# Optimization experiments

Hardware: AMD Instinct MI355X
Metric: run time of the kernel (lower is better)

The kernel has to match this reference:

```python
import jax, jax.numpy as jnp
import numpy as np
import math

D_MODEL = 2048
NUM_HEADS = 16
D_FF = 8192
HEAD_DIM = D_MODEL // NUM_HEADS
EPS = 1e-5


def _xavier(key, out_f, in_f):
    std = math.sqrt(2.0 / (in_f + out_f))
    return jax.random.normal(key, (out_f, in_f), dtype=jnp.float32) * std


def setup_inputs() -> dict:
    key = jax.random.key(0)
    ks = jax.random.split(key, 8)
    x = jax.random.normal(ks[0], (2, 2048, D_MODEL), dtype=jnp.float32)
    return {
        "x": x,
        "Wq": _xavier(ks[1], D_MODEL, D_MODEL),
        "Wk": _xavier(ks[2], D_MODEL, D_MODEL),
        "Wv": _xavier(ks[3], D_MODEL, D_MODEL),
        "Wo": _xavier(ks[4], D_MODEL, D_MODEL),
        "W1": _xavier(ks[5], D_FF, D_MODEL),
        "W2": _xavier(ks[6], D_MODEL, D_FF),
        "g1": jnp.ones((D_MODEL,), jnp.float32),
        "b1": jnp.zeros((D_MODEL,), jnp.float32),
        "g2": jnp.ones((D_MODEL,), jnp.float32),
        "b2": jnp.zeros((D_MODEL,), jnp.float32),
    }


def _ternary(w):
    # per-tensor abs-mean threshold -> {-1, 0, 1}
    abs_w = jnp.abs(w)
    thr = jnp.mean(abs_w)
    return jnp.where(abs_w > thr, jnp.sign(w), jnp.zeros_like(w))


def _tlin(x, w):
    # F.linear with ternarized weight [out, in], no bias
    return jnp.einsum("bsi,oi->bso", x, _ternary(w))


def _layernorm(x, g, b):
    mu = jnp.mean(x, axis=-1, keepdims=True)
    var = jnp.mean(jnp.square(x - mu), axis=-1, keepdims=True)
    return (x - mu) * jax.lax.rsqrt(var + EPS) * g + b


def reference(x, Wq, Wk, Wv, Wo, W1, W2, g1, b1, g2, b2):
    B, S, D = x.shape
    H, Hd = NUM_HEADS, HEAD_DIM
    q = _tlin(x, Wq).reshape(B, S, H, Hd).transpose(0, 2, 1, 3)  # bhsd
    k = _tlin(x, Wk).reshape(B, S, H, Hd).transpose(0, 2, 1, 3)
    v = _tlin(x, Wv).reshape(B, S, H, Hd).transpose(0, 2, 1, 3)
    scores = jnp.einsum("bhqd,bhkd->bhqk", q, k) / math.sqrt(Hd)
    probs = jax.nn.softmax(scores, axis=-1)
    attn = jnp.einsum("bhqk,bhkd->bhqd", probs, v)
    attn = attn.transpose(0, 2, 1, 3).reshape(B, S, D)
    attn = _tlin(attn, Wo)
    x = _layernorm(x + attn, g1, b1)  # dropout is identity in eval
    ff = _tlin(jax.nn.relu(_tlin(x, W1)), W2)
    x = _layernorm(x + ff, g2, b2)
    return x
```

## Files before the change

kernel.cpp:

```cpp
#include <hip/hip_runtime.h>
#include <hip/hip_bf16.h>

typedef __bf16 bf16_t;
typedef __bf16 bf16x8 __attribute__((ext_vector_type(8)));
typedef __bf16 bf16x4 __attribute__((ext_vector_type(4)));
typedef float f32x4 __attribute__((ext_vector_type(4)));
typedef int i32x4 __attribute__((ext_vector_type(4)));

__device__ __forceinline__ f32x4 mfma16(bf16x8 a, bf16x8 b, f32x4 c) {
  return __builtin_amdgcn_mfma_f32_16x16x32_bf16(a, b, c, 0, 0, 0);
}

__device__ __forceinline__ void gload16(const void* g, void* l) {
  __builtin_amdgcn_global_load_lds(
      (const __attribute__((address_space(1))) void*)g,
      (__attribute__((address_space(3))) void*)l, 16, 0, 0);
}

__global__ void abssum_all(const float* __restrict__ W0, const float* __restrict__ W1_,
                           const float* __restrict__ W2_, const float* __restrict__ W3,
                           const float* __restrict__ W4, const float* __restrict__ W5,
                           double* __restrict__ partial) {
  __shared__ double sd[256];
  const int w = blockIdx.y, tid = threadIdx.x;
  const float* W = (w == 0) ? W0 : (w == 1) ? W1_ : (w == 2) ? W2_ : (w == 3) ? W3 : (w == 4) ? W4 : W5;
  const int n4 = (w < 4) ? 1048576 : 4194304;
  double s = 0.0;
  for (int i = blockIdx.x * 256 + tid; i < n4; i += 262144) {
    float4 v = ((const float4*)W)[i];
    s += (double)fabsf(v.x); s += (double)fabsf(v.y);
    s += (double)fabsf(v.z); s += (double)fabsf(v.w);
  }
  sd[tid] = s; __syncthreads();
  for (int st = 128; st > 0; st >>= 1) { if (tid < st) sd[tid] += sd[tid + st]; __syncthreads(); }
  if (tid == 0) partial[w * 1024 + blockIdx.x] = sd[0];
}

__global__ void abssum_fin(const double* __restrict__ partial, double* __restrict__ sums) {
  __shared__ double sd[256];
  const int tid = threadIdx.x;
  const double* p = partial + blockIdx.x * 1024;
  double s = p[tid] + p[tid + 256] + p[tid + 512] + p[tid + 768];
  sd[tid] = s; __syncthreads();
  for (int st = 128; st > 0; st >>= 1) { if (tid < st) sd[tid] += sd[tid + st]; __syncthreads(); }
  if (tid == 0) sums[blockIdx.x] = sd[0];
}

__global__ void ternarize_k(const float* __restrict__ W, bf16_t* __restrict__ out,
                            const double* __restrict__ sum, double n) {
  const double thr = sum[0] / n;
  const int i = blockIdx.x * 256 + threadIdx.x;
  float4 v = ((const float4*)W)[i];
  bf16x4 o;
  float t;
  t = ((double)fabsf(v.x) > thr) ? (v.x > 0.f ? 1.f : -1.f) : 0.f; o[0] = (bf16_t)t;
  t = ((double)fabsf(v.y) > thr) ? (v.y > 0.f ? 1.f : -1.f) : 0.f; o[1] = (bf16_t)t;
  t = ((double)fabsf(v.z) > thr) ? (v.z > 0.f ? 1.f : -1.f) : 0.f; o[2] = (bf16_t)t;
  t = ((double)fabsf(v.w) > thr) ? (v.w > 0.f ? 1.f : -1.f) : 0.f; o[3] = (bf16_t)t;
  *(bf16x4*)&out[(size_t)i * 4] = o;
}

__global__ void split_x_k(const float* __restrict__ X, bf16_t* __restrict__ xh, bf16_t* __restrict__ xl) {
  const int i = blockIdx.x * 256 + threadIdx.x;
  float4 v = ((const float4*)X)[i];
  bf16x4 h, l;
  h[0] = (bf16_t)v.x; l[0] = (bf16_t)(v.x - (float)h[0]);
  h[1] = (bf16_t)v.y; l[1] = (bf16_t)(v.y - (float)h[1]);
  h[2] = (bf16_t)v.z; l[2] = (bf16_t)(v.z - (float)h[2]);
  h[3] = (bf16_t)v.w; l[3] = (bf16_t)(v.w - (float)h[3]);
  *(bf16x4*)&xh[(size_t)i * 4] = h;
  *(bf16x4*)&xl[(size_t)i * 4] = l;
}

template <int EPI, bool SPLITA>
__global__ __launch_bounds__(512, 2) void gemmP(
    const bf16_t* __restrict__ Ah, const bf16_t* __restrict__ Al,
    const bf16_t* __restrict__ Bw,
    void* __restrict__ C0, void* __restrict__ C1,
    int M, int N, int K) {
  constexpr int BM = SPLITA ? 64 : 128;
  constexpr int MREP = SPLITA ? 2 : 4;
  constexpr int ABUF = BM * 64;
  constexpr int BBUF = 256 * 64;
  __shared__ __align__(16) bf16_t sA[3][ABUF];
  __shared__ __align__(16) bf16_t sA2[SPLITA ? 3 : 1][SPLITA ? ABUF : 8];
  __shared__ __align__(16) bf16_t sB[3][BBUF];

  const int tid = threadIdx.x;
  const int wid = tid >> 6, lane = tid & 63, lr = lane & 15, lg = lane >> 4;
  const int wr = wid >> 2, wc = wid & 3;
  const size_t Ks = (size_t)K;

  const int nwg = gridDim.x * gridDim.y;
  const int bid0 = blockIdx.y * gridDim.x + blockIdx.x;
  const int swz = (bid0 & 7) * (nwg >> 3) + (bid0 >> 3);
  const int bx = swz % gridDim.x, by = swz / gridDim.x;
  const size_t m0 = (size_t)by * BM, n0 = (size_t)bx * 256;
  const int nt = K / 64;

  f32x4 acc[MREP][4] = {};

  auto STAGEH = [&](int bi, int kt, int half) {
    const size_t ko = (size_t)kt * 64;
    if (half == 0) {
#pragma unroll
      for (int i = 0; i < BM / 64; i++) {
        const int t = i * 512 + tid;
        const int r = t >> 3;
        const int su = (t & 7) ^ (r & 7);
        const int lo = (i * 512 + wid * 64) * 8;
        gload16(Ah + (m0 + r) * Ks + ko + su * 8, (void*)&sA[bi][lo]);
        if constexpr (SPLITA) gload16(Al + (m0 + r) * Ks + ko + su * 8, (void*)&sA2[bi][lo]);
      }
      {
        const int r = tid >> 3;
        const int su = (tid & 7) ^ (r & 7);
        gload16(Bw + (n0 + r) * Ks + ko + su * 8, (void*)&sB[bi][(wid * 64) * 8]);
      }
    } else {
#pragma unroll
      for (int i = 1; i < 4; i++) {
        const int t = i * 512 + tid;
        const int r = t >> 3;
        const int su = (t & 7) ^ (r & 7);
        gload16(Bw + (n0 + r) * Ks + ko + su * 8, (void*)&sB[bi][(i * 512 + wid * 64) * 8]);
      }
    }
  };
  auto LDA = [&](const bf16_t* base, int m, int k) -> bf16x8 {
    const int row = wr * (BM / 2) + m * 16 + lr;
    const int u = (k * 4 + lg) ^ (lr & 7);
    return *(const bf16x8*)&base[row * 64 + u * 8];
  };
  auto LDB = [&](const bf16_t* base, int n, int k) -> bf16x8 {
    const int row = wc * 64 + n * 16 + lr;
    const int u = (k * 4 + lg) ^ (lr & 7);
    return *(const bf16x8*)&base[row * 64 + u * 8];
  };

  STAGEH(0, 0, 0); STAGEH(0, 0, 1);
  STAGEH(1, 1, 0); STAGEH(1, 1, 1);
  asm volatile("s_waitcnt vmcnt(6)" ::: "memory");
  __builtin_amdgcn_s_barrier();

  int bc = 0, bs = 2;
  for (int kt = 0; kt < nt; kt++) {
    const bool pf = (kt + 2 < nt);
    bf16x8 a[MREP][2], bfr[4][2];
#pragma unroll
    for (int m = 0; m < MREP; m++)
#pragma unroll
      for (int k = 0; k < 2; k++) a[m][k] = LDA(&sA[bc][0], m, k);
    if constexpr (SPLITA) {
#pragma unroll
      for (int n = 0; n < 4; n++)
#pragma unroll
        for (int k = 0; k < 2; k++) bfr[n][k] = LDB(&sB[bc][0], n, k);
    } else {
#pragma unroll
      for (int n = 0; n < 2; n++)
#pragma unroll
        for (int k = 0; k < 2; k++) bfr[n][k] = LDB(&sB[bc][0], n, k);
    }
    if (pf) STAGEH(bs, kt + 2, 0);
    __builtin_amdgcn_s_barrier();
    asm volatile("s_waitcnt lgkmcnt(0)" ::: "memory");
    __builtin_amdgcn_sched_barrier(0);
    __builtin_amdgcn_s_setprio(1);
    if constexpr (SPLITA) {
#pragma unroll
      for (int k = 0; k < 2; k++)
#pragma unroll
        for (int m = 0; m < MREP; m++)
#pragma unroll
          for (int n = 0; n < 4; n++) acc[m][n] = mfma16(a[m][k], bfr[n][k], acc[m][n]);
    } else {
#pragma unroll
      for (int k = 0; k < 2; k++)
#pragma unroll
        for (int m = 0; m < MREP; m++)
#pragma unroll
          for (int n = 0; n < 2; n++) acc[m][n] = mfma16(a[m][k], bfr[n][k], acc[m][n]);
    }
    __builtin_amdgcn_s_setprio(0);
    __builtin_amdgcn_s_barrier();
    if constexpr (SPLITA) {
#pragma unroll
      for (int m = 0; m < MREP; m++)
#pragma unroll
        for (int k = 0; k < 2; k++) a[m][k] = LDA(&sA2[bc][0], m, k);
    } else {
#pragma unroll
      for (int n = 0; n < 2; n++)
#pragma unroll
        for (int k = 0; k < 2; k++) bfr[n + 2][k] = LDB(&sB[bc][0], n + 2, k);
    }
    if (pf) STAGEH(bs, kt + 2, 1);
    if (kt + 1 < nt) {
      if (pf) asm volatile("s_waitcnt vmcnt(6)" ::: "memory");
      else    asm volatile("s_waitcnt vmcnt(0)" ::: "memory");
    }
    __builtin_amdgcn_s_barrier();
    asm volatile("s_waitcnt lgkmcnt(0)" ::: "memory");
    __builtin_amdgcn_sched_barrier(0);
    __builtin_amdgcn_s_setprio(1);
    if constexpr (SPLITA) {
#pragma unroll
      for (int k = 0; k < 2; k++)
#pragma unroll
        for (int m = 0; m < MREP; m++)
#pragma unroll
          for (int n = 0; n < 4; n++) acc[m][n] = mfma16(a[m][k], bfr[n][k], acc[m][n]);
    } else {
#pragma unroll
      for (int k = 0; k < 2; k++)
#pragma unroll
        for (int m = 0; m < MREP; m++)
#pragma unroll
          for (int n = 0; n < 2; n++) acc[m][n + 2] = mfma16(a[m][k], bfr[n + 2][k], acc[m][n + 2]);
    }
    __builtin_amdgcn_s_setprio(0);
    __builtin_amdgcn_s_barrier();
    bc = (bc + 1 == 3) ? 0 : bc + 1;
    bs = (bs + 1 == 3) ? 0 : bs + 1;
  }

  const int row0 = (int)m0 + wr * (BM / 2), colb = (int)n0 + wc * 64;
#pragma unroll
  for (int m = 0; m < MREP; m++)
#pragma unroll
    for (int n = 0; n < 4; n++)
#pragma unroll
      for (int j = 0; j < 4; j++) {
        const int r = row0 + m * 16 + lg * 4 + j;
        const int c = colb + n * 16 + lr;
        const float v = acc[m][n][j];
        if constexpr (EPI == 0) {
          bf16_t hi = (bf16_t)v;
          ((bf16_t*)C0)[(size_t)r * N + c] = hi;
          ((bf16_t*)C1)[(size_t)r * N + c] = (bf16_t)(v - (float)hi);
        } else if constexpr (EPI == 1) {
          const int bb = r >> 11, ss = r & 2047;
          ((bf16_t*)C0)[((size_t)bb * 2048 + c) * 2048 + ss] = (bf16_t)v;
        } else if constexpr (EPI == 2) {
          ((float*)C0)[(size_t)r * N + c] = v;
        } else {
          ((bf16_t*)C0)[(size_t)r * N + c] = (bf16_t)fmaxf(v, 0.f);
        }
      }
  (void)M;
}

__global__ __launch_bounds__(256, 2) void attn_k(
    const bf16_t* __restrict__ qh, const bf16_t* __restrict__ ql,
    const bf16_t* __restrict__ kh, const bf16_t* __restrict__ kl,
    const bf16_t* __restrict__ vT, bf16_t* __restrict__ out) {
  __shared__ __align__(16) bf16_t sKh[2 * 8192];
  __shared__ __align__(16) bf16_t sKl[2 * 8192];
  __shared__ __align__(16) bf16_t plds[4][1168];

  const int fid = blockIdx.y * 16 + blockIdx.x;
  const int qt = fid >> 5;
  const int bh = (fid & 7) * 4 + ((fid >> 3) & 3);
  const int b = bh >> 4, h = bh & 15;
  const int wv = threadIdx.x >> 6, lane = threadIdx.x & 63, lr = lane & 15, lg = lane >> 4;
  const size_t tok0 = (size_t)b * 2048 + qt * 128 + wv * 16;
  bf16_t* pw = &plds[wv][0];

  auto STAGE = [&](int bufi, int kv0n) {
#pragma unroll
    for (int i = 0; i < 4; i++) {
      const int tt = wv * 4 + i;
      const int r = tt * 4 + (lane >> 4);
      const int ce = ((lane & 15) ^ (r & 7)) * 8;
      const size_t gofs = ((size_t)b * 2048 + kv0n + r) * 4096 + h * 128 + ce;
      gload16(kh + gofs, (void*)&sKh[bufi * 8192 + tt * 512]);
      gload16(kl + gofs, (void*)&sKl[bufi * 8192 + tt * 512]);
    }
  };

  bf16x8 qhf[2][4], qlf[2][4];
#pragma unroll
  for (int t = 0; t < 2; t++) {
    const bf16_t* qp = qh + (tok0 + t * 64 + lr) * 4096 + h * 128 + lg * 8;
    const bf16_t* qp2 = ql + (tok0 + t * 64 + lr) * 4096 + h * 128 + lg * 8;
#pragma unroll
    for (int ks = 0; ks < 4; ks++) {
      qhf[t][ks] = *(const bf16x8*)(qp + ks * 32);
      qlf[t][ks] = *(const bf16x8*)(qp2 + ks * 32);
    }
  }
  f32x4 oacc[2][8] = {};
  float mrun[2] = {-1e30f, -1e30f};
  float lrun[2] = {0.f, 0.f};
  const bf16_t* vbase = vT + ((size_t)b * 2048 + h * 128) * 2048;
  const float sc = 0.08838834764831845f;
  const int swz8 = 2 * (lr & 7);

  STAGE(0, 0);
  for (int c = 0; c < 32; c++) {
    const int kv0 = c * 64;
    if (c + 1 < 32) {
      STAGE((c + 1) & 1, kv0 + 64);
      asm volatile("s_waitcnt vmcnt(8)" ::: "memory");
    } else {
      asm volatile("s_waitcnt vmcnt(0)" ::: "memory");
    }
    __builtin_amdgcn_s_barrier();

    const int bufo = (c & 1) * 8192;
    f32x4 s[2][4] = {};
    __builtin_amdgcn_s_setprio(1);
#pragma unroll
    for (int nb = 0; nb < 4; nb++) {
      const int rbase = bufo + (nb * 16 + lr) * 128;
#pragma unroll
      for (int ks = 0; ks < 4; ks++) {
        const int u = (((ks * 4 + lg) ^ (lr & 7)) * 8);
        bf16x8 kf = *(const bf16x8*)&sKh[rbase + u];
        bf16x8 kg = *(const bf16x8*)&sKl[rbase + u];
        s[0][nb] = mfma16(kf, qhf[0][ks], s[0][nb]);
        s[1][nb] = mfma16(kf, qhf[1][ks], s[1][nb]);
        s[0][nb] = mfma16(kf, qlf[0][ks], s[0][nb]);
        s[1][nb] = mfma16(kf, qlf[1][ks], s[1][nb]);
        s[0][nb] = mfma16(kg, qhf[0][ks], s[0][nb]);
        s[1][nb] = mfma16(kg, qhf[1][ks], s[1][nb]);
      }
    }
    __builtin_amdgcn_s_setprio(0);

    bf16x8 pfr[2][2];
    float resc[2];
    bool skip[2];
#pragma unroll
    for (int t = 0; t < 2; t++) {
#pragma unroll
      for (int nb = 0; nb < 4; nb++) s[t][nb] *= sc;
      f32x4 m4 = __builtin_elementwise_max(
          __builtin_elementwise_max(s[t][0], s[t][1]),
          __builtin_elementwise_max(s[t][2], s[t][3]));
      float mx = fmaxf(fmaxf(m4[0], m4[1]), fmaxf(m4[2], m4[3]));
      mx = fmaxf(mx, __shfl_xor(mx, 16));
      mx = fmaxf(mx, __shfl_xor(mx, 32));
      skip[t] = (__all(mx <= mrun[t] + 8.f) != 0);
      float rs_ = 1.f;
      if (!skip[t]) {
        const float mnew = fmaxf(mrun[t], mx);
        rs_ = __expf(mrun[t] - mnew);
        mrun[t] = mnew;
      }
      resc[t] = rs_;
      float ls = 0.f;
#pragma unroll
      for (int nb = 0; nb < 4; nb++) {
        bf16x4 pk;
#pragma unroll
        for (int j = 0; j < 4; j++) {
          const float p = __expf(s[t][nb][j] - mrun[t]);
          ls += p;
          pk[j] = (bf16_t)p;
        }
        const int s8 = (4 * nb + lg) ^ swz8;
        *(bf16x4*)&pw[lr * 72 + s8 * 4] = pk;
      }
      ls += __shfl_xor(ls, 16);
      ls += __shfl_xor(ls, 32);
      lrun[t] = lrun[t] * rs_ + ls;
      asm volatile("s_waitcnt lgkmcnt(0)" ::: "memory");
      __builtin_amdgcn_sched_barrier(0);
#pragma unroll
      for (int kc = 0; kc < 2; kc++) {
        const int se = (8 * kc + 2 * lg) ^ swz8;
        pfr[t][kc] = *(const bf16x8*)&pw[lr * 72 + se * 4];
      }
    }
    if (!skip[0]) {
#pragma unroll
      for (int dt = 0; dt < 8; dt++) oacc[0][dt] *= resc[0];
    }
    if (!skip[1]) {
#pragma unroll
      for (int dt = 0; dt < 8; dt++) oacc[1][dt] *= resc[1];
    }

    const bf16_t* vp = vbase + kv0 + lg * 8;
    __builtin_amdgcn_s_setprio(1);
#pragma unroll
    for (int dt = 0; dt < 8; dt++) {
      const bf16_t* vr = vp + (size_t)(dt * 16 + lr) * 2048;
      bf16x8 v0 = *(const bf16x8*)(vr);
      bf16x8 v1 = *(const bf16x8*)(vr + 32);
      oacc[0][dt] = mfma16(v0, pfr[0][0], oacc[0][dt]);
      oacc[1][dt] = mfma16(v0, pfr[1][0], oacc[1][dt]);
      oacc[0][dt] = mfma16(v1, pfr[0][1], oacc[0][dt]);
      oacc[1][dt] = mfma16(v1, pfr[1][1], oacc[1][dt]);
    }
    __builtin_amdgcn_s_setprio(0);
    asm volatile("" ::: "memory");
    __builtin_amdgcn_s_barrier();
  }

  {
    bf16_t* ep = &sKh[wv * 2176];
    const int q = lane >> 2, c4 = lane & 3;
    const int qs = 2 * (q & 7);
#pragma unroll
    for (int t = 0; t < 2; t++) {
      const float inv = 1.f / lrun[t];
#pragma unroll
      for (int dt = 0; dt < 8; dt++) {
        bf16x4 pk;
#pragma unroll
        for (int j = 0; j < 4; j++) pk[j] = (bf16_t)(oacc[t][dt][j] * inv);
        const int s5 = (4 * dt + lg) ^ swz8;
        *(bf16x4*)&ep[lr * 136 + s5 * 4] = pk;
      }
      asm volatile("s_waitcnt lgkmcnt(0)" ::: "memory");
      __builtin_amdgcn_sched_barrier(0);
      bf16_t* orow = out + (tok0 + t * 64 + q) * 2048 + h * 128 + c4 * 32;
#pragma unroll
      for (int i = 0; i < 4; i++) {
        const int se = (c4 * 8 + 2 * i) ^ qs;
        bf16x8 vv = *(const bf16x8*)&ep[q * 136 + se * 4];
        *(bf16x8*)(orow + i * 8) = vv;
      }
      asm volatile("s_waitcnt lgkmcnt(0)" ::: "memory");
    }
  }
}

__global__ __launch_bounds__(256) void ln_k(
    const float* __restrict__ X, const float* __restrict__ R,
    const float* __restrict__ G, const float* __restrict__ Bt,
    float* __restrict__ O32, bf16_t* __restrict__ O16) {
  const int t = blockIdx.x, tid = threadIdx.x;
  const float4* xp = (const float4*)(X + (size_t)t * 2048);
  const float4* rp = (const float4*)(R + (size_t)t * 2048);
  float4 v0 = xp[tid], w0 = rp[tid];
  float4 v1 = xp[tid + 256], w1 = rp[tid + 256];
  v0.x += w0.x; v0.y += w0.y; v0.z += w0.z; v0.w += w0.w;
  v1.x += w1.x; v1.y += w1.y; v1.z += w1.z; v1.w += w1.w;
  float sum = v0.x + v0.y + v0.z + v0.w + v1.x + v1.y + v1.z + v1.w;
  float sq = v0.x * v0.x + v0.y * v0.y + v0.z * v0.z + v0.w * v0.w +
             v1.x * v1.x + v1.y * v1.y + v1.z * v1.z + v1.w * v1.w;
  for (int d = 1; d < 64; d <<= 1) { sum += __shfl_xor(sum, d); sq += __shfl_xor(sq, d); }
  __shared__ float s1[4], s2[4];
  const int wv = tid >> 6, lane = tid & 63;
  if (lane == 0) { s1[wv] = sum; s2[wv] = sq; }
  __syncthreads();
  const float tot = s1[0] + s1[1] + s1[2] + s1[3];
  const float tsq = s2[0] + s2[1] + s2[2] + s2[3];
  const float mu = tot * (1.f / 2048.f);
  const float var = tsq * (1.f / 2048.f) - mu * mu;
  const float rs = 1.f / sqrtf(var + 1e-5f);
  const float4* gp = (const float4*)G;
  const float4* bp = (const float4*)Bt;
  float4 g0 = gp[tid], g1v = gp[tid + 256], b0 = bp[tid], b1v = bp[tid + 256];
  float4 o0, o1;
  o0.x = (v0.x - mu) * rs * g0.x + b0.x; o0.y = (v0.y - mu) * rs * g0.y + b0.y;
  o0.z = (v0.z - mu) * rs * g0.z + b0.z; o0.w = (v0.w - mu) * rs * g0.w + b0.w;
  o1.x = (v1.x - mu) * rs * g1v.x + b1v.x; o1.y = (v1.y - mu) * rs * g1v.y + b1v.y;
  o1.z = (v1.z - mu) * rs * g1v.z + b1v.z; o1.w = (v1.w - mu) * rs * g1v.w + b1v.w;
  ((float4*)(O32 + (size_t)t * 2048))[tid] = o0;
  ((float4*)(O32 + (size_t)t * 2048))[tid + 256] = o1;
  if (O16) {
    bf16x4 h0, h1;
    h0[0] = (bf16_t)o0.x; h0[1] = (bf16_t)o0.y; h0[2] = (bf16_t)o0.z; h0[3] = (bf16_t)o0.w;
    h1[0] = (bf16_t)o1.x; h1[1] = (bf16_t)o1.y; h1[2] = (bf16_t)o1.z; h1[3] = (bf16_t)o1.w;
    *(bf16x4*)&O16[(size_t)t * 2048 + tid * 4] = h0;
    *(bf16x4*)&O16[(size_t)t * 2048 + 1024 + tid * 4] = h1;
  }
}

extern "C" void kernel_launch(void* const* d_in, const int* in_sizes, int n_in,
                              void* d_out, int out_size, void* d_ws, size_t ws_size,
                              hipStream_t stream) {
  const float* x  = (const float*)d_in[0];
  const float* Wq = (const float*)d_in[1];
  const float* Wk = (const float*)d_in[2];
  const float* Wv = (const float*)d_in[3];
  const float* Wo = (const float*)d_in[4];
  const float* W1 = (const float*)d_in[5];
  const float* W2 = (const float*)d_in[6];
  const float* g1 = (const float*)d_in[7];
  const float* b1 = (const float*)d_in[8];
  const float* g2 = (const float*)d_in[9];
  const float* b2 = (const float*)d_in[10];
  float* out = (float*)d_out;
  char* ws = (char*)d_ws;

  constexpr size_t SZB = (size_t)4096 * 2048 * 2;
  bf16_t* xh  = (bf16_t*)(ws + 0 * SZB);
  bf16_t* xl  = (bf16_t*)(ws + 1 * SZB);
  bf16_t* qkh = (bf16_t*)(ws + 2 * SZB);
  bf16_t* qkl = (bf16_t*)(ws + 4 * SZB);
  bf16_t* vt  = (bf16_t*)(ws + 6 * SZB);
  bf16_t* at  = (bf16_t*)(ws + 7 * SZB);
  float* o32  = (float*)(ws + 8 * SZB);
  bf16_t* wt  = (bf16_t*)(ws + 8 * SZB + (size_t)4096 * 2048 * 4);
  double* red = (double*)(ws + 8 * SZB + (size_t)4096 * 2048 * 4 + (size_t)8192 * 2048 * 2);
  double* sums = red + 8192;
  float* h1 = (float*)ws;
  bf16_t* h1b = qkh;
  bf16_t* f1 = (bf16_t*)(ws + 4 * SZB);
  float* g32 = o32;
  (void)in_sizes; (void)n_in; (void)out_size; (void)ws_size;

  abssum_all<<<dim3(1024, 6), 256, 0, stream>>>(Wq, Wk, Wv, Wo, W1, W2, red);
  abssum_fin<<<6, 256, 0, stream>>>(red, sums);
  split_x_k<<<8192, 256, 0, stream>>>(x, xh, xl);

  ternarize_k<<<4096, 256, 0, stream>>>(Wq, wt, sums + 0, 4194304.0);
  ternarize_k<<<4096, 256, 0, stream>>>(Wk, wt + 4194304, sums + 1, 4194304.0);
  gemmP<0, true><<<dim3(16, 64), 512, 0, stream>>>(xh, xl, wt, qkh, qkl, 4096, 4096, 2048);
  ternarize_k<<<4096, 256, 0, stream>>>(Wv, wt, sums + 2, 4194304.0);
  gemmP<1, false><<<dim3(8, 32), 512, 0, stream>>>(xh, nullptr, wt, vt, nullptr, 4096, 2048, 2048);
  attn_k<<<dim3(16, 32), 256, 0, stream>>>(qkh, qkl, qkh + 2048, qkl + 2048, vt, at);
  ternarize_k<<<4096, 256, 0, stream>>>(Wo, wt, sums + 3, 4194304.0);
  gemmP<2, false><<<dim3(8, 32), 512, 0, stream>>>(at, nullptr, wt, o32, nullptr, 4096, 2048, 2048);
  ln_k<<<4096, 256, 0, stream>>>(x, o32, g1, b1, h1, h1b);
  ternarize_k<<<16384, 256, 0, stream>>>(W1, wt, sums + 4, 16777216.0);
  gemmP<3, false><<<dim3(32, 32), 512, 0, stream>>>(h1b, nullptr, wt, f1, nullptr, 4096, 8192, 2048);
  ternarize_k<<<16384, 256, 0, stream>>>(W2, wt, sums + 5, 16777216.0);
  gemmP<2, false><<<dim3(8, 32), 512, 0, stream>>>(f1, nullptr, wt, g32, nullptr, 4096, 2048, 8192);
  ln_k<<<4096, 256, 0, stream>>>(h1, g32, g2, b2, out, nullptr);
}
```

Measured before the change: 893.1 us.

## Stream K-low from global in attention, raise occupancy, batch four ternarizations

The attention kernel stops staging the low-order K half in LDS and reads it straight from global memory inside the QK loop. This frees LDS so the launch bound can go from 2 to 3 blocks per CU, and the P scratch is re-laid-out per tile with one wait shared by both tiles. The four square weight ternarizations are merged into a single launch writing to separate workspace slices. The cost is uncoalesced, latency-exposed global loads of K-low in the inner MFMA loop, plus possible register pressure from the tighter launch bound.

```diff
diff --git a/kernel.cpp b/kernel.cpp
--- a/kernel.cpp
+++ b/kernel.cpp
@@ -46,6 +46,23 @@
   if (tid == 0) sums[blockIdx.x] = sd[0];
 }
 
+__global__ void ternarize4(const float* __restrict__ W0, const float* __restrict__ W1_,
+                           const float* __restrict__ W2_, const float* __restrict__ W3,
+                           bf16_t* __restrict__ out, const double* __restrict__ sums) {
+  const int w = blockIdx.x >> 12;
+  const float* W = (w == 0) ? W0 : (w == 1) ? W1_ : (w == 2) ? W2_ : W3;
+  const double thr = sums[w] / 4194304.0;
+  const int i = (blockIdx.x & 4095) * 256 + threadIdx.x;
+  float4 v = ((const float4*)W)[i];
+  bf16x4 o;
+  float t;
+  t = ((double)fabsf(v.x) > thr) ? (v.x > 0.f ? 1.f : -1.f) : 0.f; o[0] = (bf16_t)t;
+  t = ((double)fabsf(v.y) > thr) ? (v.y > 0.f ? 1.f : -1.f) : 0.f; o[1] = (bf16_t)t;
+  t = ((double)fabsf(v.z) > thr) ? (v.z > 0.f ? 1.f : -1.f) : 0.f; o[2] = (bf16_t)t;
+  t = ((double)fabsf(v.w) > thr) ? (v.w > 0.f ? 1.f : -1.f) : 0.f; o[3] = (bf16_t)t;
+  *(bf16x4*)&out[(size_t)w * 4194304 + (size_t)i * 4] = o;
+}
+
 __global__ void ternarize_k(const float* __restrict__ W, bf16_t* __restrict__ out,
                             const double* __restrict__ sum, double n) {
   const double thr = sum[0] / n;
@@ -251,13 +268,12 @@
   (void)M;
 }
 
-__global__ __launch_bounds__(256, 2) void attn_k(
+__global__ __launch_bounds__(256, 3) void attn_k(
     const bf16_t* __restrict__ qh, const bf16_t* __restrict__ ql,
     const bf16_t* __restrict__ kh, const bf16_t* __restrict__ kl,
     const bf16_t* __restrict__ vT, bf16_t* __restrict__ out) {
   __shared__ __align__(16) bf16_t sKh[2 * 8192];
-  __shared__ __align__(16) bf16_t sKl[2 * 8192];
-  __shared__ __align__(16) bf16_t plds[4][1168];
+  __shared__ __align__(16) bf16_t plds[4][2048];
 
   const int fid = blockIdx.y * 16 + blockIdx.x;
   const int qt = fid >> 5;
@@ -275,7 +291,6 @@
       const int ce = ((lane & 15) ^ (r & 7)) * 8;
       const size_t gofs = ((size_t)b * 2048 + kv0n + r) * 4096 + h * 128 + ce;
       gload16(kh + gofs, (void*)&sKh[bufi * 8192 + tt * 512]);
-      gload16(kl + gofs, (void*)&sKl[bufi * 8192 + tt * 512]);
     }
   };
 
@@ -302,7 +317,7 @@
     const int kv0 = c * 64;
     if (c + 1 < 32) {
       STAGE((c + 1) & 1, kv0 + 64);
-      asm volatile("s_waitcnt vmcnt(8)" ::: "memory");
+      asm volatile("s_waitcnt vmcnt(4)" ::: "memory");
     } else {
       asm volatile("s_waitcnt vmcnt(0)" ::: "memory");
     }
@@ -314,11 +329,12 @@
 #pragma unroll
     for (int nb = 0; nb < 4; nb++) {
       const int rbase = bufo + (nb * 16 + lr) * 128;
+      const bf16_t* klrow = kl + ((size_t)b * 2048 + kv0 + nb * 16 + lr) * 4096 + h * 128 + lg * 8;
 #pragma unroll
       for (int ks = 0; ks < 4; ks++) {
         const int u = (((ks * 4 + lg) ^ (lr & 7)) * 8);
         bf16x8 kf = *(const bf16x8*)&sKh[rbase + u];
-        bf16x8 kg = *(const bf16x8*)&sKl[rbase + u];
+        bf16x8 kg = *(const bf16x8*)(klrow + ks * 32);
         s[0][nb] = mfma16(kf, qhf[0][ks], s[0][nb]);
         s[1][nb] = mfma16(kf, qhf[1][ks], s[1][nb]);
         s[0][nb] = mfma16(kf, qlf[0][ks], s[0][nb]);
@@ -329,7 +345,6 @@
     }
     __builtin_amdgcn_s_setprio(0);
 
-    bf16x8 pfr[2][2];
     float resc[2];
     bool skip[2];
 #pragma unroll
@@ -361,19 +376,22 @@
           pk[j] = (bf16_t)p;
         }
         const int s8 = (4 * nb + lg) ^ swz8;
-        *(bf16x4*)&pw[lr * 72 + s8 * 4] = pk;
+        *(bf16x4*)&pw[t * 1024 + lr * 64 + s8 * 4] = pk;
       }
       ls += __shfl_xor(ls, 16);
       ls += __shfl_xor(ls, 32);
       lrun[t] = lrun[t] * rs_ + ls;
-      asm volatile("s_waitcnt lgkmcnt(0)" ::: "memory");
-      __builtin_amdgcn_sched_barrier(0);
+    }
+    asm volatile("s_waitcnt lgkmcnt(0)" ::: "memory");
+    __builtin_amdgcn_sched_barrier(0);
+    bf16x8 pfr[2][2];
+#pragma unroll
+    for (int t = 0; t < 2; t++)
 #pragma unroll
       for (int kc = 0; kc < 2; kc++) {
         const int se = (8 * kc + 2 * lg) ^ swz8;
-        pfr[t][kc] = *(const bf16x8*)&pw[lr * 72 + se * 4];
-      }
-    }
+        pfr[t][kc] = *(const bf16x8*)&pw[t * 1024 + lr * 64 + se * 4];
+      }
     if (!skip[0]) {
 #pragma unroll
       for (int dt = 0; dt < 8; dt++) oacc[0][dt] *= resc[0];
@@ -509,15 +527,12 @@
   abssum_all<<<dim3(1024, 6), 256, 0, stream>>>(Wq, Wk, Wv, Wo, W1, W2, red);
   abssum_fin<<<6, 256, 0, stream>>>(red, sums);
   split_x_k<<<8192, 256, 0, stream>>>(x, xh, xl);
-
-  ternarize_k<<<4096, 256, 0, stream>>>(Wq, wt, sums + 0, 4194304.0);
-  ternarize_k<<<4096, 256, 0, stream>>>(Wk, wt + 4194304, sums + 1, 4194304.0);
+  ternarize4<<<16384, 256, 0, stream>>>(Wq, Wk, Wv, Wo, wt, sums);
+
   gemmP<0, true><<<dim3(16, 64), 512, 0, stream>>>(xh, xl, wt, qkh, qkl, 4096, 4096, 2048);
-  ternarize_k<<<4096, 256, 0, stream>>>(Wv, wt, sums + 2, 4194304.0);
-  gemmP<1, false><<<dim3(8, 32), 512, 0, stream>>>(xh, nullptr, wt, vt, nullptr, 4096, 2048, 2048);
+  gemmP<1, false><<<dim3(8, 32), 512, 0, stream>>>(xh, nullptr, wt + 8388608, vt, nullptr, 4096, 2048, 2048);
   attn_k<<<dim3(16, 32), 256, 0, stream>>>(qkh, qkl, qkh + 2048, qkl + 2048, vt, at);
-  ternarize_k<<<4096, 256, 0, stream>>>(Wo, wt, sums + 3, 4194304.0);
-  gemmP<2, false><<<dim3(8, 32), 512, 0, stream>>>(at, nullptr, wt, o32, nullptr, 4096, 2048, 2048);
+  gemmP<2, false><<<dim3(8, 32), 512, 0, stream>>>(at, nullptr, wt + 12582912, o32, nullptr, 4096, 2048, 2048);
   ln_k<<<4096, 256, 0, stream>>>(x, o32, g1, b1, h1, h1b);
   ternarize_k<<<16384, 256, 0, stream>>>(W1, wt, sums + 4, 16777216.0);
   gemmP<3, false><<<dim3(32, 32), 512, 0, stream>>>(h1b, nullptr, wt, f1, nullptr, 4096, 8192, 2048);
```

After: 1.221 ms. +36.7%, slower.
